# Performance work log

Hardware: AMD Instinct MI355X
Metric: run time of the kernel (lower is better)

The kernel has to match this reference:

```python
import jax, jax.numpy as jnp
import numpy as np

B, N, M, D = 8, 4096, 4096, 128


def _cdist(x, y):
    # Euclidean distance via gram trick (matches torch.cdist p=2 math)
    # x: (B,N,D), y: (B,M,D) -> (B,N,M)
    x2 = jnp.sum(x * x, axis=-1)  # (B,N)
    y2 = jnp.sum(y * y, axis=-1)  # (B,M)
    xy = jnp.einsum('bnd,bmd->bnm', x, y)  # (B,N,M)
    sq = x2[:, :, None] + y2[:, None, :] - 2.0 * xy
    return jnp.sqrt(jnp.maximum(sq, 0.0))


def setup_inputs() -> dict:
    key = jax.random.key(0)
    k1, k2 = jax.random.split(key)
    predicted_set = jax.random.normal(k1, (B, N, D), dtype=jnp.float32)
    target_set = jax.random.normal(k2, (B, M, D), dtype=jnp.float32)
    return {"predicted_set": predicted_set, "target_set": target_set}


def reference(predicted_set, target_set):
    pairwise = _cdist(predicted_set, target_set)       # (B,N,M)
    forward_distance = jnp.min(pairwise, axis=1)        # (B,M)  (min over predicted points)
    backward_distance = jnp.min(pairwise, axis=0)       # (N,M)  (min over BATCH, as in original code)
    # reduction = 'mean'
    return jnp.mean(forward_distance) + jnp.mean(backward_distance)
```

## Files before the change

kernel.cpp:

```cpp
#include <hip/hip_runtime.h>
#include <hip/hip_fp8.h>

#define BB 8
#define NN 4096
#define MM 4096
#define DD 128

typedef float f32x4  __attribute__((ext_vector_type(4)));
typedef float f32x16 __attribute__((ext_vector_type(16)));
typedef int   i32x4  __attribute__((ext_vector_type(4)));
typedef int   i32x8  __attribute__((ext_vector_type(8)));


typedef const __attribute__((address_space(1))) unsigned int* gas_ptr;
typedef __attribute__((address_space(3))) unsigned int* las_ptr;
static __device__ __forceinline__ void gload_lds16(const unsigned char* g,
                                                   unsigned char* l) {
    __builtin_amdgcn_global_load_lds((gas_ptr)g, (las_ptr)l, 16, 0, 0);
}

__global__ __launch_bounds__(256)
void prep_all(const float* __restrict__ x, const float* __restrict__ y,
              unsigned char* __restrict__ xq, unsigned char* __restrict__ yq,
              float* __restrict__ x2, float* __restrict__ y2,
              unsigned int* __restrict__ fwd, float* __restrict__ bsum,
              float* __restrict__ fsum, unsigned int* __restrict__ counter) {
    __shared__ i32x4 lbuf[256];

    const int tid  = threadIdx.x;
    const int g    = blockIdx.x;
    const int gtid = g * 256 + tid;
    if (gtid < BB * MM) fwd[gtid] = 0x7f800000u;
    if (gtid == 0) { *bsum = 0.0f; *fsum = 0.0f; *counter = 0u; }

    const int rl = tid >> 3;
    const int c  = tid & 7;

    const float* src;
    unsigned char* dst;
    float* sq;
    float sgn;
    int row;
    if (g < 1024) {
        src = x; dst = xq + (size_t)g * 4096; sq = x2; sgn = 1.0f;
        row = g * 32 + rl;
    } else {
        src = y; dst = yq + (size_t)(g - 1024) * 4096; sq = y2; sgn = -1.0f;
        row = (g - 1024) * 32 + rl;
    }

    const f32x4* base = (const f32x4*)(src + (size_t)row * DD + c * 16);
    f32x4 v[4];
    #pragma unroll
    for (int j = 0; j < 4; ++j) v[j] = base[j];

    float s = 0.0f;
    #pragma unroll
    for (int j = 0; j < 4; ++j)
        s += v[j].x * v[j].x + v[j].y * v[j].y + v[j].z * v[j].z + v[j].w * v[j].w;

    i32x4 d;
    #pragma unroll
    for (int j = 0; j < 4; ++j) {
        unsigned int dj = (unsigned int)__builtin_amdgcn_cvt_pk_fp8_f32(
            sgn * v[j].x, sgn * v[j].y, 0, false);
        dj = (unsigned int)__builtin_amdgcn_cvt_pk_fp8_f32(
            sgn * v[j].z, sgn * v[j].w, (int)dj, true);
        d[j] = (int)dj;
    }

    const int lds_off = (c >> 2) * 2048 + ((c >> 1) & 1) * 1024
                      + rl * 32 + (c & 1) * 16;
    *(i32x4*)((char*)lbuf + lds_off) = d;

    #pragma unroll
    for (int m = 4; m; m >>= 1) s += __shfl_xor(s, m, 64);
    if (c == 0) sq[row] = 0.5f * s;

    __syncthreads();
    *(i32x4*)(dst + (size_t)tid * 16) = lbuf[tid];
}

__global__ __launch_bounds__(256, 3)
void chamfer_main(const unsigned char* __restrict__ xq, const unsigned char* __restrict__ yq,
                  const float* __restrict__ x2, const float* __restrict__ y2,
                  unsigned int* __restrict__ fwd, float* __restrict__ bpart) {
    __shared__ float x2s[BB][128];
    __shared__ float y2s[BB][64];
    __shared__ unsigned int fbuf[BB][64];
    __shared__ unsigned char ybuf[2][8192];
    __shared__ float red[4];

    const int tid   = threadIdx.x;
    const int lane  = tid & 63;
    const int wave  = tid >> 6;
    const int lhalf = lane >> 5;
    const int l31   = lane & 31;

    const int id  = blockIdx.x;
    const int xcd = id & 7;
    const int j   = id >> 3;
    const int nb  = (xcd >> 1) * 8 + (j & 7);
    const int mb  = (xcd & 1) * 32 + (j >> 3);
    const int n0b = nb * 128;
    const int n0w = n0b + wave * 32;
    const int m0  = mb * 64;

    const size_t laneoff = (size_t)lhalf * 1024 + (size_t)l31 * 32;
    const unsigned char* xbase = xq + (size_t)(n0w >> 5) * 4096 + laneoff;

    const size_t ysw = (size_t)(wave >> 1) * 2048 + (size_t)(wave & 1) * 1024
                     + ((size_t)lhalf << 4) + (size_t)l31 * 32;
    const unsigned char* ybase = yq + (size_t)(2 * mb) * 4096 + ysw;
    const int rb0 = l31 * 16 + lhalf * 1024;

    auto stage_y = [&](int b, int s) {
        const unsigned char* gsrc = ybase + ((size_t)b << 19);
        gload_lds16(gsrc,        &ybuf[s][wave * 1024]);
        gload_lds16(gsrc + 4096, &ybuf[s][4096 + wave * 1024]);
    };

    i32x4 fx[2][2][2];
    auto loadx = [&](int b, int s) {
        const unsigned char* xb = xbase + ((size_t)b << 19);
        #pragma unroll
        for (int i = 0; i < 2; ++i)
            #pragma unroll
            for (int hh = 0; hh < 2; ++hh)
                fx[s][i][hh] = *(const i32x4*)(xb + i * 2048 + hh * 16);
    };

    stage_y(0, 0);
    loadx(0, 0);
    for (int i = tid; i < BB * 128; i += 256)
        x2s[i >> 7][i & 127] = x2[(size_t)(i >> 7) * NN + n0b + (i & 127)];
    for (int i = tid; i < BB * 64; i += 256) {
        y2s[i >> 6][i & 63] = y2[(size_t)(i >> 6) * MM + m0 + (i & 63)];
        ((unsigned int*)fbuf)[i] = 0x7f800000u;
    }
    __syncthreads();

    const float INF = __builtin_inff();
    float bmin[2][16];
    #pragma unroll
    for (int t = 0; t < 2; ++t)
        #pragma unroll
        for (int r = 0; r < 16; ++r) bmin[t][r] = INF;

    #pragma unroll 2
    for (int b = 0; b < BB; ++b) {
        const int cur = b & 1;
        if (b < BB - 1) {
            stage_y(b + 1, cur ^ 1);
            loadx(b + 1, cur ^ 1);
        }

        float y2v[2];
        y2v[0] = y2s[b][l31];
        y2v[1] = y2s[b][32 + l31];
        f32x16 acc[2];
        #pragma unroll
        for (int q = 0; q < 4; ++q) {
            f32x4 xv = *(const f32x4*)&x2s[b][wave * 32 + lhalf * 4 + q * 8];
            #pragma unroll
            for (int t = 0; t < 2; ++t)
                #pragma unroll
                for (int e = 0; e < 4; ++e)
                    acc[t][q * 4 + e] = xv[e] + y2v[t];
        }

        #pragma unroll
        for (int i = 0; i < 2; ++i) {
            i32x8 av = __builtin_shufflevector(fx[cur][i][0], fx[cur][i][1],
                                               0, 1, 2, 3, 4, 5, 6, 7);
            #pragma unroll
            for (int t = 0; t < 2; ++t) {
                const unsigned char* yb = &ybuf[cur][t * 4096 + i * 2048 + rb0];
                i32x4 lo = *(const i32x4*)(yb);
                i32x4 hi = *(const i32x4*)(yb + 512);
                i32x8 bv = __builtin_shufflevector(lo, hi, 0, 1, 2, 3, 4, 5, 6, 7);
                acc[t] = __builtin_amdgcn_mfma_scale_f32_32x32x64_f8f6f4(
                    av, bv, acc[t], 0, 0, 0, 127, 0, 127);
            }
        }

        float fm[2] = {INF, INF};
        #pragma unroll
        for (int t = 0; t < 2; ++t)
            #pragma unroll
            for (int r = 0; r < 16; ++r) {
                bmin[t][r] = fminf(bmin[t][r], acc[t][r]);
                fm[t]      = fminf(fm[t], acc[t][r]);
            }
        #pragma unroll
        for (int t = 0; t < 2; ++t)
            atomicMin(&fbuf[b][t * 32 + l31],
                      __float_as_uint(fmaxf(fm[t], 0.0f)));

        __syncthreads();
    }

    for (int i = tid; i < BB * 64; i += 256)
        atomicMin(&fwd[(size_t)(i >> 6) * MM + m0 + (i & 63)], fbuf[i >> 6][i & 63]);

    float s = 0.0f;
    #pragma unroll
    for (int t = 0; t < 2; ++t)
        #pragma unroll
        for (int r = 0; r < 16; ++r)
            s += sqrtf(2.0f * fmaxf(bmin[t][r], 0.0f));
    #pragma unroll
    for (int off = 32; off; off >>= 1) s += __shfl_down(s, off, 64);
    if (lane == 0) red[wave] = s;
    __syncthreads();
    if (tid == 0) bpart[id] = red[0] + red[1] + red[2] + red[3];
}

__global__ __launch_bounds__(256)
void finalize_kernel(const unsigned int* __restrict__ fwd,
                     const float* __restrict__ bpart,
                     float* __restrict__ bsum, float* __restrict__ fsum,
                     unsigned int* __restrict__ counter, float* __restrict__ out) {
    __shared__ float redf[4], redb[4];
    __shared__ int isLast;
    const int tid = threadIdx.x, lane = tid & 63, wave = tid >> 6;
    const int gtid = blockIdx.x * 256 + tid;
    uint4 u = ((const uint4*)fwd)[gtid];
    float sf = sqrtf(2.0f * __uint_as_float(u.x)) + sqrtf(2.0f * __uint_as_float(u.y)) +
               sqrtf(2.0f * __uint_as_float(u.z)) + sqrtf(2.0f * __uint_as_float(u.w));
    float sb = (gtid < 2048) ? bpart[gtid] : 0.0f;
    #pragma unroll
    for (int off = 32; off; off >>= 1) {
        sf += __shfl_down(sf, off, 64);
        sb += __shfl_down(sb, off, 64);
    }
    if (lane == 0) { redf[wave] = sf; redb[wave] = sb; }
    __syncthreads();
    if (tid == 0) {
        atomicAdd(fsum, redf[0] + redf[1] + redf[2] + redf[3]);
        atomicAdd(bsum, redb[0] + redb[1] + redb[2] + redb[3]);
        __threadfence();
        unsigned int c = atomicAdd(counter, 1u);
        isLast = (c == gridDim.x - 1) ? 1 : 0;
        if (isLast) {
            __threadfence();
            float fs = __hip_atomic_load(fsum, __ATOMIC_RELAXED,
                                         __HIP_MEMORY_SCOPE_AGENT);
            float bs = __hip_atomic_load(bsum, __ATOMIC_RELAXED,
                                         __HIP_MEMORY_SCOPE_AGENT);
            out[0] = fs / (float)(BB * MM) + bs / ((float)NN * (float)MM);
        }
    }
}

extern "C" void kernel_launch(void* const* d_in, const int* in_sizes, int n_in,
                              void* d_out, int out_size, void* d_ws, size_t ws_size,
                              hipStream_t stream) {
    const float* x = (const float*)d_in[0];
    const float* y = (const float*)d_in[1];
    float* out = (float*)d_out;

    char* w = (char*)d_ws;
    unsigned char* xq = (unsigned char*)(w);
    unsigned char* yq = (unsigned char*)(w + 4194304);
    float*    x2 = (float*)(w + 8388608);
    float*    y2 = (float*)(w + 8519680);
    unsigned int* fwd = (unsigned int*)(w + 8650752);
    float*    bpart = (float*)(w + 8781824);
    float*    bsum = (float*)(w + 8798208);
    float*    fsum = (float*)(w + 8798212);
    unsigned int* counter = (unsigned int*)(w + 8798216);

    prep_all<<<2048, 256, 0, stream>>>(x, y, xq, yq, x2, y2,
                                       fwd, bsum, fsum, counter);
    chamfer_main<<<2048, 256, 0, stream>>>(xq, yq, x2, y2, fwd, bpart);
    finalize_kernel<<<32, 256, 0, stream>>>(fwd, bpart, bsum, fsum, counter, out);
}
```

Baseline: 116.8 us.

## Double block tile height and stage all batches of Y into LDS upfront

Each block now runs 512 threads and covers 256 predicted rows instead of 128, so every Y tile held in LDS is reused by twice as many rows and the grid shrinks to 1024 blocks. All 8 batch slices of the Y tile are loaded into LDS at kernel start rather than double-buffered per batch. This removes the per-batch __syncthreads and the staging inside the loop. In exchange, LDS use per block rises to roughly 76 KB, which limits blocks per CU, and the full Y load latency is exposed once at the start instead of overlapped with compute.

Measured after the change: 139.9 us. +19.8%, slower.

```diff
diff --git a/kernel.cpp b/kernel.cpp
--- a/kernel.cpp
+++ b/kernel.cpp
@@ -81,15 +81,15 @@
     *(i32x4*)(dst + (size_t)tid * 16) = lbuf[tid];
 }
 
-__global__ __launch_bounds__(256, 3)
+__global__ __launch_bounds__(512, 4)
 void chamfer_main(const unsigned char* __restrict__ xq, const unsigned char* __restrict__ yq,
                   const float* __restrict__ x2, const float* __restrict__ y2,
                   unsigned int* __restrict__ fwd, float* __restrict__ bpart) {
-    __shared__ float x2s[BB][128];
+    __shared__ float x2s[BB][256];
     __shared__ float y2s[BB][64];
     __shared__ unsigned int fbuf[BB][64];
-    __shared__ unsigned char ybuf[2][8192];
-    __shared__ float red[4];
+    __shared__ unsigned char ybuf[BB][8192];
+    __shared__ float red[8];
 
     const int tid   = threadIdx.x;
     const int lane  = tid & 63;
@@ -100,25 +100,23 @@
     const int id  = blockIdx.x;
     const int xcd = id & 7;
     const int j   = id >> 3;
-    const int nb  = (xcd >> 1) * 8 + (j & 7);
-    const int mb  = (xcd & 1) * 32 + (j >> 3);
-    const int n0b = nb * 128;
+    const int nb  = (xcd >> 1) * 4 + (j & 3);
+    const int mb  = (xcd & 1) * 32 + (j >> 2);
+    const int n0b = nb * 256;
     const int n0w = n0b + wave * 32;
     const int m0  = mb * 64;
 
     const size_t laneoff = (size_t)lhalf * 1024 + (size_t)l31 * 32;
     const unsigned char* xbase = xq + (size_t)(n0w >> 5) * 4096 + laneoff;
 
-    const size_t ysw = (size_t)(wave >> 1) * 2048 + (size_t)(wave & 1) * 1024
-                     + ((size_t)lhalf << 4) + (size_t)l31 * 32;
-    const unsigned char* ybase = yq + (size_t)(2 * mb) * 4096 + ysw;
-    const int rb0 = l31 * 16 + lhalf * 1024;
-
-    auto stage_y = [&](int b, int s) {
-        const unsigned char* gsrc = ybase + ((size_t)b << 19);
-        gload_lds16(gsrc,        &ybuf[s][wave * 1024]);
-        gload_lds16(gsrc + 4096, &ybuf[s][4096 + wave * 1024]);
-    };
+    const size_t ysw = (size_t)(wave >> 2) * 4096 + (size_t)((wave >> 1) & 1) * 2048
+                     + (size_t)(wave & 1) * 1024 + (size_t)l31 * 32
+                     + (size_t)lhalf * 16;
+    const unsigned char* ybase = yq + (size_t)mb * 8192 + ysw;
+
+    #pragma unroll
+    for (int b = 0; b < BB; ++b)
+        gload_lds16(ybase + ((size_t)b << 19), &ybuf[b][wave * 1024]);
 
     i32x4 fx[2][2][2];
     auto loadx = [&](int b, int s) {
@@ -129,12 +127,12 @@
             for (int hh = 0; hh < 2; ++hh)
                 fx[s][i][hh] = *(const i32x4*)(xb + i * 2048 + hh * 16);
     };
-
-    stage_y(0, 0);
     loadx(0, 0);
-    for (int i = tid; i < BB * 128; i += 256)
-        x2s[i >> 7][i & 127] = x2[(size_t)(i >> 7) * NN + n0b + (i & 127)];
-    for (int i = tid; i < BB * 64; i += 256) {
+
+    for (int i = tid; i < BB * 256; i += 512)
+        x2s[i >> 8][i & 255] = x2[(size_t)(i >> 8) * NN + n0b + (i & 255)];
+    {
+        int i = tid;
         y2s[i >> 6][i & 63] = y2[(size_t)(i >> 6) * MM + m0 + (i & 63)];
         ((unsigned int*)fbuf)[i] = 0x7f800000u;
     }
@@ -146,14 +144,13 @@
     for (int t = 0; t < 2; ++t)
         #pragma unroll
         for (int r = 0; r < 16; ++r) bmin[t][r] = INF;
+
+    const int rb0 = lhalf * 1024 + l31 * 16;
 
     #pragma unroll 2
     for (int b = 0; b < BB; ++b) {
         const int cur = b & 1;
-        if (b < BB - 1) {
-            stage_y(b + 1, cur ^ 1);
-            loadx(b + 1, cur ^ 1);
-        }
+        if (b < BB - 1) loadx(b + 1, cur ^ 1);
 
         float y2v[2];
         y2v[0] = y2s[b][l31];
@@ -175,7 +172,7 @@
                                                0, 1, 2, 3, 4, 5, 6, 7);
             #pragma unroll
             for (int t = 0; t < 2; ++t) {
-                const unsigned char* yb = &ybuf[cur][t * 4096 + i * 2048 + rb0];
+                const unsigned char* yb = &ybuf[b][t * 4096 + i * 2048 + rb0];
                 i32x4 lo = *(const i32x4*)(yb);
                 i32x4 hi = *(const i32x4*)(yb + 512);
                 i32x8 bv = __builtin_shufflevector(lo, hi, 0, 1, 2, 3, 4, 5, 6, 7);
@@ -196,12 +193,13 @@
         for (int t = 0; t < 2; ++t)
             atomicMin(&fbuf[b][t * 32 + l31],
                       __float_as_uint(fmaxf(fm[t], 0.0f)));
-
-        __syncthreads();
-    }
-
-    for (int i = tid; i < BB * 64; i += 256)
+    }
+    __syncthreads();
+
+    {
+        int i = tid;
         atomicMin(&fwd[(size_t)(i >> 6) * MM + m0 + (i & 63)], fbuf[i >> 6][i & 63]);
+    }
 
     float s = 0.0f;
     #pragma unroll
@@ -213,7 +211,9 @@
     for (int off = 32; off; off >>= 1) s += __shfl_down(s, off, 64);
     if (lane == 0) red[wave] = s;
     __syncthreads();
-    if (tid == 0) bpart[id] = red[0] + red[1] + red[2] + red[3];
+    if (tid == 0)
+        bpart[id] = red[0] + red[1] + red[2] + red[3]
+                  + red[4] + red[5] + red[6] + red[7];
 }
 
 __global__ __launch_bounds__(256)
@@ -228,7 +228,7 @@
     uint4 u = ((const uint4*)fwd)[gtid];
     float sf = sqrtf(2.0f * __uint_as_float(u.x)) + sqrtf(2.0f * __uint_as_float(u.y)) +
                sqrtf(2.0f * __uint_as_float(u.z)) + sqrtf(2.0f * __uint_as_float(u.w));
-    float sb = (gtid < 2048) ? bpart[gtid] : 0.0f;
+    float sb = (gtid < 1024) ? bpart[gtid] : 0.0f;
     #pragma unroll
     for (int off = 32; off; off >>= 1) {
         sf += __shfl_down(sf, off, 64);
@@ -273,6 +273,6 @@
 
     prep_all<<<2048, 256, 0, stream>>>(x, y, xq, yq, x2, y2,
                                        fwd, bsum, fsum, counter);
-    chamfer_main<<<2048, 256, 0, stream>>>(xq, yq, x2, y2, fwd, bpart);
+    chamfer_main<<<1024, 512, 0, stream>>>(xq, yq, x2, y2, fwd, bpart);
     finalize_kernel<<<32, 256, 0, stream>>>(fwd, bpart, bsum, fsum, counter, out);
 }
```
